# Performance work log

Hardware: AMD Instinct MI355X
Metric: run time of the kernel (lower is better)

The kernel has to match this reference:

```python
import jax, jax.numpy as jnp
import numpy as np

NUM_CLASSES = 40
EOS_COEF = 0.1
IGNORE = 255
W_CLASS, W_MASK, W_DICE = 2.0, 5.0, 5.0
EPS = 1e-8


def setup_inputs() -> dict:
    key = jax.random.key(0)
    k1, k2, k3, k4 = jax.random.split(key, 4)
    B, Q, H, W = 4, 100, 256, 256
    pred_logits = jax.random.normal(k1, (B, Q, NUM_CLASSES + 1), dtype=jnp.float32)
    pred_masks = jax.random.normal(k2, (B, Q, H, W), dtype=jnp.float32)
    targets = jax.random.randint(k3, (B, H, W), 0, NUM_CLASSES)
    ign = jax.random.uniform(k4, (B, H, W)) < 0.05
    targets = jnp.where(ign, IGNORE, targets).astype(jnp.int32)
    return {"pred_logits": pred_logits, "pred_masks": pred_masks, "targets": targets}


def reference(pred_logits, pred_masks, targets):
    B, Q, _ = pred_logits.shape
    C = NUM_CLASSES
    f32 = jnp.float32
    valid = targets != IGNORE                      # [B,H,W]
    tgt_safe = jnp.where(valid, targets, 0)        # in-range for indexing

    # ---- loss_labels: pixel->query assignment, per-query mode label ----
    # sigmoid is monotone, so argmax over queries of raw logits == argmax of sigmoid
    assign = jnp.argmax(pred_masks, axis=1)        # [B,H,W]
    b_idx = jnp.broadcast_to(jnp.arange(B)[:, None, None], targets.shape)
    # counts[b,q,c] = #valid pixels assigned to query q with label c
    counts = jnp.zeros((B, Q, C), f32).at[b_idx, assign, tgt_safe].add(valid.astype(f32))
    has_pix = counts.sum(-1) > 0                   # [B,Q]
    # mode = argmax of counts (ties -> smallest class, matching torch.mode)
    target_classes = jnp.where(has_pix, jnp.argmax(counts, axis=-1), C)  # [B,Q]

    logp = jax.nn.log_softmax(pred_logits, axis=-1)                      # [B,Q,C+1]
    nll = -jnp.take_along_axis(logp, target_classes[..., None], axis=-1)[..., 0]
    empty_weight = jnp.ones(C + 1, f32).at[-1].set(EOS_COEF)
    # ignore_index = num_classes in the CE over classes
    ce = jnp.where(target_classes != C, nll * empty_weight[target_classes], 0.0)
    p = jnp.exp(-ce)
    loss_ce = jnp.mean((1.0 - p) ** 2 * ce)

    # ---- loss_masks: per-pixel CE over queries + per-class dice ----
    logp_pix = jax.nn.log_softmax(pred_masks, axis=1)                    # [B,Q,H,W]
    nll_pix = -jnp.take_along_axis(logp_pix, tgt_safe[:, None], axis=1)[:, 0]  # [B,H,W]
    n_valid = valid.astype(f32).sum()
    ce_mask = jnp.sum(jnp.where(valid, nll_pix, 0.0)) / jnp.maximum(n_valid, 1.0)

    sig = jax.nn.sigmoid(pred_masks)                                     # [B,Q,H,W]
    tmask = (targets[:, None] == jnp.arange(C)[None, :, None, None]).astype(f32)  # [B,C,H,W]
    vm = valid[:, None].astype(f32)                                      # [B,1,H,W]
    inter = jnp.einsum('bqhw,bchw->bqc', sig, tmask * vm)                # numerator uses valid mask
    src_sum = sig.sum(axis=(2, 3))                                       # [B,Q]
    tsum = tmask.sum(axis=(2, 3))                                        # [B,C]
    dice = 2.0 * inter / (src_sum[:, :, None] + tsum[:, None, :] + EPS)  # [B,Q,C]
    present = tsum.sum(axis=0) > 0                                       # [C]
    dice_loss = jnp.sum(jnp.where(present, 1.0 - dice.mean(axis=(0, 1)), 0.0)) / C

    combined = W_MASK * ce_mask + W_DICE * dice_loss
    return W_CLASS * loss_ce + combined
```

## Files before the change

kernel.cpp:

```cpp
#include <hip/hip_runtime.h>

constexpr int B = 4, Q = 100, C = 40, Cp1 = 41, HW = 65536;

constexpr int FBLKS = 512;

constexpr int WS_WORDS = 32562;

typedef __attribute__((ext_vector_type(8))) short short8;
typedef __attribute__((ext_vector_type(4))) float f32x4;

__device__ __forceinline__ short f2bf(float f) {
    unsigned u = __float_as_uint(f);
    u += 0x7FFF + ((u >> 16) & 1);
    return (short)(u >> 16);
}

__global__ void kZ(unsigned* __restrict__ ws, int n) {
    int i = blockIdx.x * blockDim.x + threadIdx.x;
    for (; i < n; i += gridDim.x * blockDim.x) ws[i] = 0u;
}

__global__ __launch_bounds__(256) void kF(const float* __restrict__ masks,
                                          const int* __restrict__ targets,
                                          unsigned* __restrict__ counts,
                                          unsigned* __restrict__ tsum,
                                          float* __restrict__ ce_sum,
                                          unsigned* __restrict__ n_valid,
                                          float* __restrict__ inter_ext) {
    __shared__ __align__(16) short tileS[2][16 * 512];
    __shared__ float inter_lds[Q * Cp1];
    __shared__ __align__(8) unsigned char tgt8[512];
    __shared__ unsigned ts_local[C];
    __shared__ float cred[4];
    __shared__ unsigned vred[4];

    const int tid = threadIdx.x;
    const int l = tid & 63, w = tid >> 6;
    const int m = l & 15, quad = l >> 4;

    const int blk = blockIdx.x;
    const int b = blk >> 7;
    const int seg = blk & 127;
    const int p0 = seg * 512 + 2 * tid;

    const int2 tg = *(const int2*)(targets + (size_t)b * HW + p0);
    const int tg0 = tg.x, tg1 = tg.y;
    *(unsigned short*)&tgt8[2 * tid] =
        (unsigned short)((tg0 & 255) | ((tg1 & 255) << 8));
    if (tid < C) ts_local[tid] = 0u;
    #pragma unroll
    for (int i = 0; i < 17; ++i) {
        int idx = tid + i * 256;
        if (idx < Q * Cp1) inter_lds[idx] = 0.f;
    }

    const float* mp = masks + (size_t)b * Q * HW + p0;

    float m20 = -INFINITY, m21 = -INFINITY;
    float s0 = 0.f, s1 = 0.f, xt0 = 0.f, xt1 = 0.f;
    int am0 = 0, am1 = 0;

    const int cv = (w == 2 && m == 8) ? 255 : (w * 16 + m);

    for (int qt = 0; qt < 7; ++qt) {
        char* tbq = (char*)(&tileS[qt & 1][0]);
        const int nu = (qt == 6) ? 4 : 16;

        float2 vv[16];
        #pragma unroll
        for (int u = 0; u < 16; ++u)
            if (u < nu) vv[u] = *(const float2*)(mp + (size_t)(qt * 16 + u) * HW);

        #pragma unroll
        for (int u = 0; u < 16; ++u)
            if (u < nu) {
                const int q = qt * 16 + u;
                const float v0 = vv[u].x, v1 = vv[u].y;
                s0 += __expf(v0);
                s1 += __expf(v1);
                am0 = (v0 > m20) ? q : am0;  m20 = fmaxf(m20, v0);
                am1 = (v1 > m21) ? q : am1;  m21 = fmaxf(m21, v1);
                xt0 = (q == tg0) ? v0 : xt0;
                xt1 = (q == tg1) ? v1 : xt1;
                const float g0 = __builtin_amdgcn_rcpf(1.f + __expf(-v0));
                const float g1 = __builtin_amdgcn_rcpf(1.f + __expf(-v1));
                const unsigned pk = (unsigned)(unsigned short)f2bf(g0) |
                                    ((unsigned)(unsigned short)f2bf(g1) << 16);
                *(unsigned*)(tbq + ((u * 1024 + 4 * tid) ^ ((u & 7) << 4))) = pk;
            }

        __syncthreads();

        if (w < 3) {
            f32x4 acc = {0.f, 0.f, 0.f, 0.f};
            #pragma unroll
            for (int kc = 0; kc < 16; ++kc) {
                const short8 av = *(const short8*)(tbq +
                    ((m * 1024 + kc * 64 + quad * 16) ^ ((m & 7) << 4)));
                const unsigned long long tw =
                    *(const unsigned long long*)&tgt8[kc * 32 + quad * 8];
                short8 bv;
                #pragma unroll
                for (int j = 0; j < 8; ++j)
                    bv[j] = ((int)((tw >> (8 * j)) & 255) == cv)
                                ? (short)0x3F80 : (short)0;
                acc = __builtin_amdgcn_mfma_f32_16x16x32_bf16(av, bv, acc,
                                                              0, 0, 0);
            }
            if (!(w == 2 && m > 8)) {
                #pragma unroll
                for (int reg = 0; reg < 4; ++reg) {
                    const int q = qt * 16 + quad * 4 + reg;
                    if (q < 100)
                        atomicAdd(&inter_lds[q * Cp1 + w * 16 + m], acc[reg]);
                }
            }
        }
    }

    float ce = 0.f;
    unsigned nv = 0u;
    if (tg0 != 255) {
        ce += __logf(s0) - xt0; nv++;
        atomicAdd(&counts[((size_t)b * Q + am0) * C + tg0], 1u);
        atomicAdd(&ts_local[tg0], 1u);
    }
    if (tg1 != 255) {
        ce += __logf(s1) - xt1; nv++;
        atomicAdd(&counts[((size_t)b * Q + am1) * C + tg1], 1u);
        atomicAdd(&ts_local[tg1], 1u);
    }
    for (int off = 32; off; off >>= 1) {
        ce += __shfl_xor(ce, off);
        nv += __shfl_xor(nv, off);
    }
    if (l == 0) { cred[w] = ce; vred[w] = nv; }
    __syncthreads();
    if (tid == 0) {
        atomicAdd(ce_sum, cred[0] + cred[1] + cred[2] + cred[3]);
        atomicAdd(n_valid, vred[0] + vred[1] + vred[2] + vred[3]);
    }
    if (tid < C) {
        unsigned t = ts_local[tid];
        if (t) atomicAdd(&tsum[b * C + tid], t);
    }

    const size_t ibase = (size_t)b * Q * Cp1;
    #pragma unroll
    for (int i = 0; i < 17; ++i) {
        int idx = tid + i * 256;
        if (idx < Q * Cp1) {
            float v = inter_lds[idx];
            if (v != 0.f) atomicAdd(&inter_ext[ibase + idx], v);
        }
    }
}

__global__ __launch_bounds__(1024) void kC(const float* __restrict__ logits,
                                           const unsigned* __restrict__ counts,
                                           const unsigned* __restrict__ tsum,
                                           const float* __restrict__ inter_ext,
                                           const float* __restrict__ ce_sum,
                                           const unsigned* __restrict__ n_valid,
                                           float* __restrict__ out) {
    int tid = threadIdx.x;
    __shared__ float dice_sum[C];
    __shared__ float ssum[B * Q];
    __shared__ float wred[16];
    __shared__ float s_lce;
    if (tid < C) dice_sum[tid] = 0.f;
    if (tid < B * Q) {
        const float* r = inter_ext + (size_t)tid * Cp1;
        float t = 0.f;
        #pragma unroll
        for (int c = 0; c < Cp1; ++c) t += r[c];
        ssum[tid] = t;
    }

    float ce_acc = 0.f;
    for (int i = tid; i < B * Q; i += 1024) {
        const unsigned* cnt = counts + (size_t)i * C;
        unsigned best = 0;
        int tc = C;
        #pragma unroll
        for (int c = 0; c < C; ++c) {
            unsigned v = cnt[c];
            if (v > best) { best = v; tc = c; }
        }
        if (tc != C) {
            const float* lg = logits + (size_t)i * Cp1;
            float mm = -INFINITY, xt = 0.f;
            #pragma unroll
            for (int c = 0; c < Cp1; ++c) {
                float v = lg[c];
                mm = fmaxf(mm, v);
                if (c == tc) xt = v;
            }
            float ss = 0.f;
            #pragma unroll
            for (int c = 0; c < Cp1; ++c) ss += __expf(lg[c] - mm);
            float nll = mm + __logf(ss) - xt;
            float p = __expf(-nll);
            float om = 1.f - p;
            ce_acc += om * om * nll;
        }
    }
    for (int off = 32; off; off >>= 1) ce_acc += __shfl_xor(ce_acc, off);
    if ((tid & 63) == 0) wred[tid >> 6] = ce_acc;
    __syncthreads();
    if (tid == 0) {
        float t = 0.f;
        for (int w = 0; w < 16; ++w) t += wred[w];
        s_lce = t;
    }

    for (int i = tid; i < B * Q * C; i += 1024) {
        int bq = i / C, c = i - bq * C;
        float denom = ssum[bq] + (float)tsum[(bq / Q) * C + c] + 1e-8f;
        atomicAdd(&dice_sum[c], 2.f * inter_ext[(size_t)bq * Cp1 + c] / denom);
    }
    __syncthreads();

    if (tid == 0) {
        float dl = 0.f;
        for (int c = 0; c < C; ++c) {
            unsigned ts = tsum[c] + tsum[C + c] + tsum[2 * C + c] + tsum[3 * C + c];
            if (ts > 0) dl += 1.f - dice_sum[c] * (1.f / (B * Q));
        }
        dl *= (1.f / C);
        float ce_mask = ce_sum[0] / fmaxf((float)n_valid[0], 1.f);
        float lce = s_lce * (1.f / (B * Q));
        out[0] = 2.f * lce + 5.f * ce_mask + 5.f * dl;
    }
}

extern "C" void kernel_launch(void* const* d_in, const int* in_sizes, int n_in,
                              void* d_out, int out_size, void* d_ws, size_t ws_size,
                              hipStream_t stream) {
    const float* logits  = (const float*)d_in[0];
    const float* masks   = (const float*)d_in[1];
    const int*   targets = (const int*)d_in[2];
    float* out = (float*)d_out;

    unsigned* ws        = (unsigned*)d_ws;
    unsigned* counts    = ws;
    unsigned* tsum      = ws + 16000;
    float*    ce_sum    = (float*)(ws + 16160);
    unsigned* n_valid   = ws + 16161;
    float*    inter_ext = (float*)(ws + 16162);

    kZ<<<64, 256, 0, stream>>>(ws, WS_WORDS);
    kF<<<FBLKS, 256, 0, stream>>>(masks, targets, counts, tsum, ce_sum, n_valid,
                                  inter_ext);
    kC<<<1, 1024, 0, stream>>>(logits, counts, tsum, inter_ext, ce_sum, n_valid, out);
}
```

Baseline: 206.0 us.

## Prefetch mask tiles into LDS asynchronously and accumulate intersections with global atomics

Mask values are now staged into shared memory with global_load_lds, and the next 16-query tile is issued while the MFMA intersection phase runs, so load latency overlaps compute. The per-block LDS intersection buffer is removed, and MFMA results are added directly into the global intersection array. This frees LDS and removes the zero/flush loops, but it sends many more contended global float atomics.

```diff
diff --git a/kernel.cpp b/kernel.cpp
--- a/kernel.cpp
+++ b/kernel.cpp
@@ -13,6 +13,12 @@
     unsigned u = __float_as_uint(f);
     u += 0x7FFF + ((u >> 16) & 1);
     return (short)(u >> 16);
+}
+
+__device__ __forceinline__ void gload16(const void* g, void* l) {
+    __builtin_amdgcn_global_load_lds(
+        (const __attribute__((address_space(1))) unsigned*)g,
+        (__attribute__((address_space(3))) unsigned*)l, 16, 0, 0);
 }
 
 __global__ void kZ(unsigned* __restrict__ ws, int n) {
@@ -27,8 +33,8 @@
                                           float* __restrict__ ce_sum,
                                           unsigned* __restrict__ n_valid,
                                           float* __restrict__ inter_ext) {
+    __shared__ __align__(16) float stageF[16 * 512];
     __shared__ __align__(16) short tileS[2][16 * 512];
-    __shared__ float inter_lds[Q * Cp1];
     __shared__ __align__(8) unsigned char tgt8[512];
     __shared__ unsigned ts_local[C];
     __shared__ float cred[4];
@@ -48,13 +54,24 @@
     *(unsigned short*)&tgt8[2 * tid] =
         (unsigned short)((tg0 & 255) | ((tg1 & 255) << 8));
     if (tid < C) ts_local[tid] = 0u;
-    #pragma unroll
-    for (int i = 0; i < 17; ++i) {
-        int idx = tid + i * 256;
-        if (idx < Q * Cp1) inter_lds[idx] = 0.f;
-    }
-
-    const float* mp = masks + (size_t)b * Q * HW + p0;
+
+    const float* mseg = masks + (size_t)b * Q * HW + seg * 512;
+
+    auto STAGE = [&](int qt) {
+        const int q0 = qt * 16 + w * 4;
+        if (q0 < 100) {
+            const float* pb = mseg + (size_t)q0 * HW;
+            char* lb = (char*)stageF + (w * 4) * 2048;
+            #pragma unroll
+            for (int j = 0; j < 8; ++j) {
+                const int u = j >> 1, half = j & 1;
+                gload16(pb + (size_t)u * HW + half * 256 + l * 4,
+                        lb + u * 2048 + half * 1024);
+            }
+        }
+    };
+
+    STAGE(0);
 
     float m20 = -INFINITY, m21 = -INFINITY;
     float s0 = 0.f, s1 = 0.f, xt0 = 0.f, xt1 = 0.f;
@@ -66,16 +83,14 @@
         char* tbq = (char*)(&tileS[qt & 1][0]);
         const int nu = (qt == 6) ? 4 : 16;
 
-        float2 vv[16];
-        #pragma unroll
-        for (int u = 0; u < 16; ++u)
-            if (u < nu) vv[u] = *(const float2*)(mp + (size_t)(qt * 16 + u) * HW);
+        __syncthreads();
 
         #pragma unroll
         for (int u = 0; u < 16; ++u)
             if (u < nu) {
                 const int q = qt * 16 + u;
-                const float v0 = vv[u].x, v1 = vv[u].y;
+                const float2 vp = *(const float2*)&stageF[u * 512 + 2 * tid];
+                const float v0 = vp.x, v1 = vp.y;
                 s0 += __expf(v0);
                 s1 += __expf(v1);
                 am0 = (v0 > m20) ? q : am0;  m20 = fmaxf(m20, v0);
@@ -90,6 +105,8 @@
             }
 
         __syncthreads();
+
+        if (qt < 6) STAGE(qt + 1);
 
         if (w < 3) {
             f32x4 acc = {0.f, 0.f, 0.f, 0.f};
@@ -112,7 +129,8 @@
                 for (int reg = 0; reg < 4; ++reg) {
                     const int q = qt * 16 + quad * 4 + reg;
                     if (q < 100)
-                        atomicAdd(&inter_lds[q * Cp1 + w * 16 + m], acc[reg]);
+                        atomicAdd(&inter_ext[(size_t)(b * Q + q) * Cp1 +
+                                             w * 16 + m], acc[reg]);
                 }
             }
         }
@@ -143,16 +161,6 @@
     if (tid < C) {
         unsigned t = ts_local[tid];
         if (t) atomicAdd(&tsum[b * C + tid], t);
-    }
-
-    const size_t ibase = (size_t)b * Q * Cp1;
-    #pragma unroll
-    for (int i = 0; i < 17; ++i) {
-        int idx = tid + i * 256;
-        if (idx < Q * Cp1) {
-            float v = inter_lds[idx];
-            if (v != 0.f) atomicAdd(&inter_ext[ibase + idx], v);
-        }
     }
 }
 
```

Measured after the change: 213.9 us. 3.8% more time.
